# Kernel tuning notes

Measured on AMD Instinct MI355X. Metric: run time of the kernel, lower is better.

The kernel has to match this reference:

```python
import jax, jax.numpy as jnp
import numpy as np

B, DM, H, M, K = 2, 256, 4, 4096, 16
DIM = DM // H  # per-head feature dim = 64


def _proj(x, W, b):
    # 1x1 Conv2d on channels-first (B, C, M, K): pointwise linear over channels
    return jnp.einsum('oi,bimk->bomk', W, x) + b[None, :, None, None]


def setup_inputs() -> dict:
    rng = jax.random.key(0)
    ks = jax.random.split(rng, 11)
    s = 1.0 / np.sqrt(DM)
    return {
        'query': jax.random.normal(ks[0], (B, DM, M, 1), jnp.float32),
        'key':   jax.random.normal(ks[1], (B, DM, M, K), jnp.float32),
        'value': jax.random.normal(ks[2], (B, DM, M, K), jnp.float32),
        'Wq': jax.random.normal(ks[3], (DM, DM), jnp.float32) * s,
        'bq': jax.random.normal(ks[4], (DM,), jnp.float32) * 0.01,
        'Wk': jax.random.normal(ks[5], (DM, DM), jnp.float32) * s,
        'bk': jax.random.normal(ks[6], (DM,), jnp.float32) * 0.01,
        'Wv': jax.random.normal(ks[7], (DM, DM), jnp.float32) * s,
        'bv': jax.random.normal(ks[8], (DM,), jnp.float32) * 0.01,
        'Wm': jax.random.normal(ks[9], (DM, DM), jnp.float32) * s,
        'bm': jax.random.normal(ks[10], (DM,), jnp.float32) * 0.01,
    }


def reference(query, key, value, Wq, bq, Wk, bk, Wv, bv, Wm, bm):
    # project; torch view(B, dim, heads, -1) on channels-first => channel c -> (d=c//H, h=c%H)
    q = _proj(query, Wq, bq).reshape(B, DIM, H, M)          # (b, d, h, m)
    k = _proj(key,   Wk, bk).reshape(B, DIM, H, M, K)        # (b, d, h, m, k)
    v = _proj(value, Wv, bv).reshape(B, DIM, H, M, K)
    scores = jnp.einsum('bfhm,bfhmk->bhmk', q, k) / np.sqrt(DIM).astype(np.float32)
    prob = jax.nn.softmax(scores, axis=-1)                   # softmax over kn neighbors
    x = jnp.einsum('bhmk,bdhmk->bdhm', prob, v)              # (b, d, h, m)
    out = _proj(x.reshape(B, DM, M, 1), Wm, bm)              # merge 1x1 conv
    prob_sum = jnp.sum(prob, axis=1)                         # (b, m, k)
    return out, prob_sum
```

## Files before the change

### kernel.cpp

```cpp
#include <hip/hip_runtime.h>
#include <stdint.h>

#define DM_ 256
#define H_ 4
#define M_ 4096
#define KN_ 16
#define B_ 2
#define MK_ (M_*KN_)

typedef __attribute__((ext_vector_type(8))) short short8;
typedef __attribute__((ext_vector_type(4))) float f32x4;
typedef __attribute__((ext_vector_type(4))) unsigned short u16x4;

static __device__ __forceinline__ unsigned short f2bf(float x) {
  union { float f; uint32_t u; } v; v.f = x;
  uint32_t u = v.u + (0x7FFFu + ((v.u >> 16) & 1u));
  return (unsigned short)(u >> 16);
}
static __device__ __forceinline__ float u2f(uint32_t u) {
  union { uint32_t u; float f; } v; v.u = u; return v.f;
}

static __device__ __forceinline__ int swz512(int col, int kbyte) {
  int f = ((col >> 2) & 7) ^ ((col & 1) << 2);
  return (col << 9) + (kbyte ^ (f << 4));
}

__global__ void prep2(const float* __restrict__ Wq, const float* __restrict__ bq,
                      const float* __restrict__ Wk, const float* __restrict__ Wv,
                      const float* __restrict__ bv, const float* __restrict__ Wm,
                      const float* __restrict__ bm,
                      unsigned short* __restrict__ W2T, unsigned short* __restrict__ Wmv,
                      float* __restrict__ qb2, float* __restrict__ btot) {
  int t = blockIdx.x * 512 + threadIdx.x;
  if (t < 262144) {
    int j = t & 7, lane = (t >> 3) & 63, rowblk = (t >> 9) & 63, kstep = t >> 15;
    int row = rowblk * 16 + (lane & 15);
    int k = kstep * 32 + (lane >> 4) * 8 + j;
    int h = row >> 8, c = row & 255;
    float v = 0.f;
#pragma unroll 8
    for (int d = 0; d < 64; ++d) v += Wq[(4 * d + h) * 256 + k] * Wk[(4 * d + h) * 256 + c];
    W2T[t] = f2bf(v);
  } else if (t < 524288) {
    int e = t - 262144;
    int j = e & 7, lane = (e >> 3) & 63, rowblk = (e >> 9) & 15, kstep = e >> 13;
    int o = rowblk * 16 + (lane & 15);
    int kidx = kstep * 32 + (lane >> 4) * 8 + j;
    int c = kidx >> 2, h = kidx & 3;
    float v = 0.f;
#pragma unroll 8
    for (int d = 0; d < 64; ++d) v += Wm[o * 256 + 4 * d + h] * Wv[(4 * d + h) * 256 + c];
    Wmv[e] = f2bf(v);
  } else if (t < 525312) {
    int r = t - 524288; int h = r >> 8, c = r & 255;
    float v = 0.f;
#pragma unroll 8
    for (int d = 0; d < 64; ++d) v += bq[4 * d + h] * Wk[(4 * d + h) * 256 + c];
    qb2[r] = v;
  } else if (t < 525568) {
    int o = t - 525312;
    float v = bm[o];
#pragma unroll 8
    for (int c2 = 0; c2 < 256; ++c2) v += Wm[o * 256 + c2] * bv[c2];
    btot[o] = v;
  }
}

__global__ __launch_bounds__(512)
void qw_gemm(const float* __restrict__ query, const unsigned short* __restrict__ W2T,
             const float* __restrict__ qb2, unsigned short* __restrict__ qWbuf) {
  __shared__ unsigned short Xl[32 * 256];
  const int tid = threadIdx.x;
  const int lane = tid & 63, wid = tid >> 6;
  const int wr = wid >> 1, wc = wid & 1;
  const int mt = blockIdx.x & 127;
  const int rt = (blockIdx.x >> 7) & 3;
  const int b = blockIdx.x >> 9;
  const int m0 = mt * 32;
  const float* Xb = query + (size_t)b * DM_ * M_ + m0;
  const int c4 = 4 * (tid & 7);
  const int ch0 = 4 * (tid >> 3);
  float4 f[4];
#pragma unroll
  for (int i = 0; i < 4; ++i) f[i] = *(const float4*)(Xb + (size_t)(ch0 + i) * M_ + c4);
#pragma unroll
  for (int j = 0; j < 4; ++j) {
    u16x4 u = { f2bf(((const float*)&f[0])[j]), f2bf(((const float*)&f[1])[j]),
                f2bf(((const float*)&f[2])[j]), f2bf(((const float*)&f[3])[j]) };
    *(u16x4*)((char*)Xl + swz512(c4 + j, 2 * ch0)) = u;
  }
  __syncthreads();
  f32x4 acc[4] = {};
  const int bcol = wc * 16 + (lane & 15);
  const int rdk = 16 * (lane >> 4);
  short8 a_cur[4], a_nxt[4];
#pragma unroll
  for (int fi = 0; fi < 4; ++fi)
    a_cur[fi] = *(const short8*)(W2T + (size_t)(((rt * 16 + wr * 4 + fi) * 64 + lane) * 8));
#pragma unroll
  for (int kgs = 0; kgs < 8; ++kgs) {
    if (kgs < 7) {
#pragma unroll
      for (int fi = 0; fi < 4; ++fi)
        a_nxt[fi] = *(const short8*)(W2T + (size_t)((((kgs + 1) * 64 + rt * 16 + wr * 4 + fi) * 64 + lane) * 8));
    }
    short8 bb = *(const short8*)((const char*)Xl + swz512(bcol, 64 * kgs + rdk));
#pragma unroll
    for (int fi = 0; fi < 4; ++fi)
      acc[fi] = __builtin_amdgcn_mfma_f32_16x16x32_bf16(a_cur[fi], bb, acc[fi], 0, 0, 0);
#pragma unroll
    for (int fi = 0; fi < 4; ++fi) a_cur[fi] = a_nxt[fi];
  }
#pragma unroll
  for (int fi = 0; fi < 4; ++fi) {
#pragma unroll
    for (int r = 0; r < 4; ++r) {
      const int rr = rt * 256 + wr * 64 + fi * 16 + (lane >> 4) * 4 + r;
      qWbuf[(size_t)(b * 1024 + rr) * M_ + m0 + bcol] = f2bf(acc[fi][r] + qb2[rr]);
    }
  }
}

__global__ __launch_bounds__(1024, 4)
void fused_attn(const float* __restrict__ key, const float* __restrict__ value,
                const unsigned short* __restrict__ qW, const unsigned short* __restrict__ Wmv,
                const float* __restrict__ btot, float* __restrict__ out,
                float* __restrict__ psum) {
  __shared__ __align__(16) char LDS[135168];
  const int KRING = 0, QSL = 49152, SCX = 0, PVT = 49152, VRING = 81920, PROB = 131072;
  unsigned short* qsl = (unsigned short*)(LDS + QSL);
  float* ldsP = (float*)(LDS + PROB);
  const int tid = threadIdx.x;
  const int lane = tid & 63;
  const int w = tid >> 6;
  const int vb = (blockIdx.x & 7) * 64 + (blockIdx.x >> 3);
  const int b = vb >> 8;
  const int m0 = (vb & 255) * 16;
  {
    const int c = tid & 255, h = tid >> 8;
    const unsigned short* src = qW + ((size_t)(b * 1024 + h * 256 + c)) * M_ + m0;
    uint4 rv[2];
    rv[0] = *(const uint4*)(src);
    rv[1] = *(const uint4*)(src + 8);
    const unsigned short* rs = (const unsigned short*)rv;
#pragma unroll
    for (int q = 0; q < 16; ++q) {
      const int slot = (q + c) & 15;
      qsl[c * 64 + slot * 4 + h] = rs[q];
    }
  }
  __syncthreads();
  const int mp = lane >> 2;
  const int kkq = lane & 3;
  const float* ksrc = key   + (size_t)(b * 256) * 65536 + (size_t)m0 * 16 + lane * 4;
  const float* vsrc = value + (size_t)(b * 256) * 65536 + (size_t)m0 * 16 + lane * 4;
  f32x4 ps0 = {}, ps1 = {}, ps2 = {}, ps3 = {};

#define KISS(ch, slot) \
  __builtin_amdgcn_global_load_lds( \
      (const __attribute__((address_space(1))) uint32_t*)(ksrc + (size_t)(w * 16 + (ch)) * 65536), \
      (__attribute__((address_space(3))) uint32_t*)(LDS + KRING + w * 3072 + (slot) * 1024), 16, 0, 0)
#define VISS(ch, slot) \
  __builtin_amdgcn_global_load_lds( \
      (const __attribute__((address_space(1))) uint32_t*)(vsrc + (size_t)(w * 16 + (ch)) * 65536), \
      (__attribute__((address_space(3))) uint32_t*)(LDS + VRING + w * 3072 + (slot) * 1024), 16, 0, 0)
#define KCONS(i, slot, n) { \
    asm volatile("s_waitcnt vmcnt(" #n ")" ::: "memory"); \
    __builtin_amdgcn_sched_barrier(0); \
    const int c = w * 16 + (i); \
    const f32x4 kv = *(const f32x4*)(LDS + KRING + w * 3072 + (slot) * 1024 + lane * 16); \
    const uint2 qv = *(const uint2*)&qsl[c * 64 + (((mp + c) & 15)) * 4]; \
    ps0 += kv * u2f(qv.x << 16); \
    ps1 += kv * u2f(qv.x & 0xffff0000u); \
    ps2 += kv * u2f(qv.y << 16); \
    ps3 += kv * u2f(qv.y & 0xffff0000u); \
  }
  KISS(0, 0); KISS(1, 1); KISS(2, 2);
  KCONS(0, 0, 2)  KISS(3, 0);
  KCONS(1, 1, 2)  KISS(4, 1);
  KCONS(2, 2, 2)  KISS(5, 2);
  KCONS(3, 0, 2)  KISS(6, 0);
  KCONS(4, 1, 2)  KISS(7, 1);
  KCONS(5, 2, 2)  KISS(8, 2);
  KCONS(6, 0, 2)  KISS(9, 0);
  KCONS(7, 1, 2)  KISS(10, 1);
  KCONS(8, 2, 2)  KISS(11, 2);
  KCONS(9, 0, 2)  KISS(12, 0);
  KCONS(10, 1, 2) KISS(13, 1);
  KCONS(11, 2, 2) KISS(14, 2);
  KCONS(12, 0, 2) KISS(15, 0);
  KCONS(13, 1, 2)
  KCONS(14, 2, 1)
  KCONS(15, 0, 0)
  VISS(0, 0); VISS(1, 1); VISS(2, 2);
  __builtin_amdgcn_s_barrier();
  {
    char* base = LDS + SCX + w * 4096 + lane * 64;
    const int sw = (lane >> 1) & 3;
    *(f32x4*)(base + ((0 ^ sw) << 4)) = ps0;
    *(f32x4*)(base + ((1 ^ sw) << 4)) = ps1;
    *(f32x4*)(base + ((2 ^ sw) << 4)) = ps2;
    *(f32x4*)(base + ((3 ^ sw) << 4)) = ps3;
  }
  asm volatile("s_waitcnt lgkmcnt(0)" ::: "memory");
  __builtin_amdgcn_s_barrier();
  {
    const int mp2 = tid >> 6;
    const int h2 = (lane >> 4) & 3;
    const int kk = lane & 15;
    const int lanep = mp2 * 4 + (kk >> 2);
    const int slotr = h2 ^ ((lanep >> 1) & 3);
    const int off = SCX + lanep * 64 + (slotr << 4) + (kk & 3) * 4;
    float sc = 0.f;
#pragma unroll
    for (int w2 = 0; w2 < 16; ++w2) sc += *(const float*)(LDS + w2 * 4096 + off);
    sc *= 0.125f;
    float mx = sc;
    mx = fmaxf(mx, __shfl_xor(mx, 1)); mx = fmaxf(mx, __shfl_xor(mx, 2));
    mx = fmaxf(mx, __shfl_xor(mx, 4)); mx = fmaxf(mx, __shfl_xor(mx, 8));
    const float e = __expf(sc - mx);
    float sm = e;
    sm += __shfl_xor(sm, 1); sm += __shfl_xor(sm, 2);
    sm += __shfl_xor(sm, 4); sm += __shfl_xor(sm, 8);
    ldsP[(mp2 * 4 + h2) * 16 + kk] = e / sm;
  }
  asm volatile("s_waitcnt lgkmcnt(0)" ::: "memory");
  __builtin_amdgcn_s_barrier();
  const f32x4 pr0 = *(const f32x4*)&ldsP[(mp * 4 + 0) * 16 + kkq * 4];
  const f32x4 pr1 = *(const f32x4*)&ldsP[(mp * 4 + 1) * 16 + kkq * 4];
  const f32x4 pr2 = *(const f32x4*)&ldsP[(mp * 4 + 2) * 16 + kkq * 4];
  const f32x4 pr3 = *(const f32x4*)&ldsP[(mp * 4 + 3) * 16 + kkq * 4];
#define VCONS(i, slot, n) { \
    asm volatile("s_waitcnt vmcnt(" #n ")" ::: "memory"); \
    __builtin_amdgcn_sched_barrier(0); \
    const int c = w * 16 + (i); \
    const f32x4 vv = *(const f32x4*)(LDS + VRING + w * 3072 + (slot) * 1024 + lane * 16); \
    float p0 = pr0[0] * vv[0] + pr0[1] * vv[1] + pr0[2] * vv[2] + pr0[3] * vv[3]; \
    float p1 = pr1[0] * vv[0] + pr1[1] * vv[1] + pr1[2] * vv[2] + pr1[3] * vv[3]; \
    float p2 = pr2[0] * vv[0] + pr2[1] * vv[1] + pr2[2] * vv[2] + pr2[3] * vv[3]; \
    float p3 = pr3[0] * vv[0] + pr3[1] * vv[1] + pr3[2] * vv[2] + pr3[3] * vv[3]; \
    p0 += __shfl_xor(p0, 1); p0 += __shfl_xor(p0, 2); \
    p1 += __shfl_xor(p1, 1); p1 += __shfl_xor(p1, 2); \
    p2 += __shfl_xor(p2, 1); p2 += __shfl_xor(p2, 2); \
    p3 += __shfl_xor(p3, 1); p3 += __shfl_xor(p3, 2); \
    if (kkq == 0) { \
      uint2 o; \
      o.x = (uint32_t)f2bf(p0) | ((uint32_t)f2bf(p1) << 16); \
      o.y = (uint32_t)f2bf(p2) | ((uint32_t)f2bf(p3) << 16); \
      *(uint2*)(LDS + PVT + ((mp * 2048 + c * 8) ^ ((mp & 7) << 4))) = o; \
    } \
  }
  VCONS(0, 0, 2)  VISS(3, 0);
  VCONS(1, 1, 2)  VISS(4, 1);
  VCONS(2, 2, 2)  VISS(5, 2);
  VCONS(3, 0, 2)  VISS(6, 0);
  VCONS(4, 1, 2)  VISS(7, 1);
  VCONS(5, 2, 2)  VISS(8, 2);
  VCONS(6, 0, 2)  VISS(9, 0);
  VCONS(7, 1, 2)  VISS(10, 1);
  VCONS(8, 2, 2)  VISS(11, 2);
  VCONS(9, 0, 2)  VISS(12, 0);
  VCONS(10, 1, 2) VISS(13, 1);
  VCONS(11, 2, 2) VISS(14, 2);
  VCONS(12, 0, 2) VISS(15, 0);
  VCONS(13, 1, 2)
  VCONS(14, 2, 1)
  VCONS(15, 0, 0)
  asm volatile("s_waitcnt lgkmcnt(0)" ::: "memory");
  __builtin_amdgcn_s_barrier();
  {
    const int wid = tid >> 6;
    const int bcol = lane & 15;
    const int kgrp = lane >> 4;
    f32x4 acc = {};
    for (int kgs = 0; kgs < 32; ++kgs) {
      const int byte = PVT + (((bcol * 2048 + kgs * 64 + kgrp * 16)) ^ ((bcol & 7) << 4));
      const short8 bb = *(const short8*)(LDS + byte);
      const short8 a0 = *(const short8*)(Wmv + (size_t)(((kgs * 16 + wid) * 64 + lane) * 8));
      acc = __builtin_amdgcn_mfma_f32_16x16x32_bf16(a0, bb, acc, 0, 0, 0);
    }
#pragma unroll
    for (int r = 0; r < 4; ++r) {
      const int o = wid * 16 + kgrp * 4 + r;
      out[((size_t)(b * DM_ + o)) * M_ + m0 + bcol] = acc[r] + btot[o];
    }
  }
  if (tid < 256) {
    const int mp2 = tid >> 4, kk = tid & 15;
    psum[((size_t)b * M_ + m0 + mp2) * KN_ + kk] =
        ldsP[(mp2 * 4 + 0) * 16 + kk] + ldsP[(mp2 * 4 + 1) * 16 + kk] +
        ldsP[(mp2 * 4 + 2) * 16 + kk] + ldsP[(mp2 * 4 + 3) * 16 + kk];
  }
#undef KISS
#undef VISS
#undef KCONS
#undef VCONS
}

extern "C" void kernel_launch(void* const* d_in, const int* in_sizes, int n_in,
                              void* d_out, int out_size, void* d_ws, size_t ws_size,
                              hipStream_t stream) {
  const float* query = (const float*)d_in[0];
  const float* key   = (const float*)d_in[1];
  const float* value = (const float*)d_in[2];
  const float* Wq = (const float*)d_in[3];
  const float* bq = (const float*)d_in[4];
  const float* Wk = (const float*)d_in[5];
  const float* bk = (const float*)d_in[6];  (void)bk;
  const float* Wv = (const float*)d_in[7];
  const float* bv = (const float*)d_in[8];
  const float* Wm = (const float*)d_in[9];
  const float* bm = (const float*)d_in[10];
  float* out  = (float*)d_out;
  float* psum = out + (size_t)B_ * DM_ * M_;

  const size_t Wmv_off  = 524288;
  const size_t qb2_off  = 1048576;
  const size_t btot_off = 1052672;
  const size_t qW_off   = 1053696;

  unsigned short* W2T   = (unsigned short*)d_ws;
  unsigned short* Wmv   = (unsigned short*)((char*)d_ws + Wmv_off);
  float* qb2            = (float*)((char*)d_ws + qb2_off);
  float* btot           = (float*)((char*)d_ws + btot_off);
  unsigned short* qWbuf = (unsigned short*)((char*)d_ws + qW_off);

  prep2<<<dim3(1027), dim3(512), 0, stream>>>(Wq, bq, Wk, Wv, bv, Wm, bm, W2T, Wmv, qb2, btot);
  qw_gemm<<<dim3(B_ * 4 * 128), dim3(512), 0, stream>>>(query, W2T, qb2, qWbuf);
  fused_attn<<<dim3(512), dim3(1024), 0, stream>>>(key, value, qWbuf, Wmv, btot, out, psum);
}
```

Before: 109.2 us.

## Fuse query-weight GEMM into attention kernel prologue, drop qw_gemm launch

The separate qw_gemm kernel and its bf16 qW buffer in global memory are removed. Each fused_attn block now loads its own 16 query columns, converts them to bf16 in LDS, and runs the 1024x256 MFMA product against W2T directly, writing results into the qsl layout. This removes one kernel launch and the global write/read round trip of qW. In exchange each block reloads the whole W2T matrix from global/L2 without prefetch, which adds work before the key/value stream starts.

```diff
diff --git a/kernel.cpp b/kernel.cpp
--- a/kernel.cpp
+++ b/kernel.cpp
@@ -19,11 +19,6 @@
 }
 static __device__ __forceinline__ float u2f(uint32_t u) {
   union { uint32_t u; float f; } v; v.u = u; return v.f;
-}
-
-static __device__ __forceinline__ int swz512(int col, int kbyte) {
-  int f = ((col >> 2) & 7) ^ ((col & 1) << 2);
-  return (col << 9) + (kbyte ^ (f << 4));
 }
 
 __global__ void prep2(const float* __restrict__ Wq, const float* __restrict__ bq,
@@ -67,68 +62,15 @@
   }
 }
 
-__global__ __launch_bounds__(512)
-void qw_gemm(const float* __restrict__ query, const unsigned short* __restrict__ W2T,
-             const float* __restrict__ qb2, unsigned short* __restrict__ qWbuf) {
-  __shared__ unsigned short Xl[32 * 256];
-  const int tid = threadIdx.x;
-  const int lane = tid & 63, wid = tid >> 6;
-  const int wr = wid >> 1, wc = wid & 1;
-  const int mt = blockIdx.x & 127;
-  const int rt = (blockIdx.x >> 7) & 3;
-  const int b = blockIdx.x >> 9;
-  const int m0 = mt * 32;
-  const float* Xb = query + (size_t)b * DM_ * M_ + m0;
-  const int c4 = 4 * (tid & 7);
-  const int ch0 = 4 * (tid >> 3);
-  float4 f[4];
-#pragma unroll
-  for (int i = 0; i < 4; ++i) f[i] = *(const float4*)(Xb + (size_t)(ch0 + i) * M_ + c4);
-#pragma unroll
-  for (int j = 0; j < 4; ++j) {
-    u16x4 u = { f2bf(((const float*)&f[0])[j]), f2bf(((const float*)&f[1])[j]),
-                f2bf(((const float*)&f[2])[j]), f2bf(((const float*)&f[3])[j]) };
-    *(u16x4*)((char*)Xl + swz512(c4 + j, 2 * ch0)) = u;
-  }
-  __syncthreads();
-  f32x4 acc[4] = {};
-  const int bcol = wc * 16 + (lane & 15);
-  const int rdk = 16 * (lane >> 4);
-  short8 a_cur[4], a_nxt[4];
-#pragma unroll
-  for (int fi = 0; fi < 4; ++fi)
-    a_cur[fi] = *(const short8*)(W2T + (size_t)(((rt * 16 + wr * 4 + fi) * 64 + lane) * 8));
-#pragma unroll
-  for (int kgs = 0; kgs < 8; ++kgs) {
-    if (kgs < 7) {
-#pragma unroll
-      for (int fi = 0; fi < 4; ++fi)
-        a_nxt[fi] = *(const short8*)(W2T + (size_t)((((kgs + 1) * 64 + rt * 16 + wr * 4 + fi) * 64 + lane) * 8));
-    }
-    short8 bb = *(const short8*)((const char*)Xl + swz512(bcol, 64 * kgs + rdk));
-#pragma unroll
-    for (int fi = 0; fi < 4; ++fi)
-      acc[fi] = __builtin_amdgcn_mfma_f32_16x16x32_bf16(a_cur[fi], bb, acc[fi], 0, 0, 0);
-#pragma unroll
-    for (int fi = 0; fi < 4; ++fi) a_cur[fi] = a_nxt[fi];
-  }
-#pragma unroll
-  for (int fi = 0; fi < 4; ++fi) {
-#pragma unroll
-    for (int r = 0; r < 4; ++r) {
-      const int rr = rt * 256 + wr * 64 + fi * 16 + (lane >> 4) * 4 + r;
-      qWbuf[(size_t)(b * 1024 + rr) * M_ + m0 + bcol] = f2bf(acc[fi][r] + qb2[rr]);
-    }
-  }
-}
-
 __global__ __launch_bounds__(1024, 4)
 void fused_attn(const float* __restrict__ key, const float* __restrict__ value,
-                const unsigned short* __restrict__ qW, const unsigned short* __restrict__ Wmv,
+                const float* __restrict__ query, const unsigned short* __restrict__ W2T,
+                const float* __restrict__ qb2, const unsigned short* __restrict__ Wmv,
                 const float* __restrict__ btot, float* __restrict__ out,
                 float* __restrict__ psum) {
   __shared__ __align__(16) char LDS[135168];
-  const int KRING = 0, QSL = 49152, SCX = 0, PVT = 49152, VRING = 81920, PROB = 131072;
+  const int KRING = 0, QSL = 49152, SCX = 0, PVT = 49152, VRING = 81920;
+  const int QS = 81920, QB = 90112, PROB = 131072;
   unsigned short* qsl = (unsigned short*)(LDS + QSL);
   float* ldsP = (float*)(LDS + PROB);
   const int tid = threadIdx.x;
@@ -138,16 +80,39 @@
   const int b = vb >> 8;
   const int m0 = (vb & 255) * 16;
   {
-    const int c = tid & 255, h = tid >> 8;
-    const unsigned short* src = qW + ((size_t)(b * 1024 + h * 256 + c)) * M_ + m0;
-    uint4 rv[2];
-    rv[0] = *(const uint4*)(src);
-    rv[1] = *(const uint4*)(src + 8);
-    const unsigned short* rs = (const unsigned short*)rv;
-#pragma unroll
-    for (int q = 0; q < 16; ++q) {
-      const int slot = (q + c) & 15;
-      qsl[c * 64 + slot * 4 + h] = rs[q];
+    const int cp = tid >> 2, q4 = (tid & 3) * 4;
+    const float4 qv = *(const float4*)(query + (size_t)(b * DM_ + cp) * M_ + m0 + q4);
+#pragma unroll
+    for (int e = 0; e < 4; ++e) {
+      const int mq2 = q4 + e;
+      const int l = (((cp >> 3) & 3) << 4) | mq2;
+      *(unsigned short*)(LDS + QS + ((cp >> 5) * 64 + l) * 16 + (cp & 7) * 2) =
+          f2bf(((const float*)&qv)[e]);
+    }
+    ((float*)(LDS + QB))[tid] = qb2[tid];
+  }
+  __syncthreads();
+  {
+    f32x4 acc[4] = {};
+#pragma unroll
+    for (int kgs = 0; kgs < 8; ++kgs) {
+      const short8 bb = *(const short8*)(LDS + QS + kgs * 1024 + lane * 16);
+#pragma unroll
+      for (int fi = 0; fi < 4; ++fi) {
+        const short8 a0 = *(const short8*)(W2T + (size_t)(((kgs * 64 + w * 4 + fi) * 64 + lane) * 8));
+        acc[fi] = __builtin_amdgcn_mfma_f32_16x16x32_bf16(a0, bb, acc[fi], 0, 0, 0);
+      }
+    }
+    const int mq2 = lane & 15;
+#pragma unroll
+    for (int fi = 0; fi < 4; ++fi) {
+#pragma unroll
+      for (int rr = 0; rr < 4; ++rr) {
+        const int r = (w * 4 + fi) * 16 + ((lane >> 4) << 2) + rr;
+        const int h = r >> 8, c = r & 255;
+        const int slot = (mq2 + c) & 15;
+        qsl[c * 64 + slot * 4 + h] = f2bf(acc[fi][rr] + ((const float*)(LDS + QB))[r]);
+      }
     }
   }
   __syncthreads();
@@ -318,15 +283,13 @@
   const size_t Wmv_off  = 524288;
   const size_t qb2_off  = 1048576;
   const size_t btot_off = 1052672;
-  const size_t qW_off   = 1053696;
 
   unsigned short* W2T   = (unsigned short*)d_ws;
   unsigned short* Wmv   = (unsigned short*)((char*)d_ws + Wmv_off);
   float* qb2            = (float*)((char*)d_ws + qb2_off);
   float* btot           = (float*)((char*)d_ws + btot_off);
-  unsigned short* qWbuf = (unsigned short*)((char*)d_ws + qW_off);
 
   prep2<<<dim3(1027), dim3(512), 0, stream>>>(Wq, bq, Wk, Wv, bv, Wm, bm, W2T, Wmv, qb2, btot);
-  qw_gemm<<<dim3(B_ * 4 * 128), dim3(512), 0, stream>>>(query, W2T, qb2, qWbuf);
-  fused_attn<<<dim3(512), dim3(1024), 0, stream>>>(key, value, qWbuf, Wmv, btot, out, psum);
-}
+  fused_attn<<<dim3(512), dim3(1024), 0, stream>>>(key, value, query, W2T, qb2,
+                                                   Wmv, btot, out, psum);
+}
```

Result: faster. 96.17 us (-12.0%).
